# Optimization experiments

Hardware: AMD Instinct MI355X
Metric: run time of the kernel (lower is better)

The kernel has to match this reference:

```python
import jax, jax.numpy as jnp
import numpy as np

N_V, N_H, T, B = 1024, 512, 128, 256


def setup_inputs() -> dict:
    key = jax.random.key(0)
    k = jax.random.split(key, 3)
    v_data = (jax.random.uniform(k[0], (N_V, T, B)) < 0.5).astype(jnp.float32)  # binary visibles
    W = 0.01 * jax.random.normal(k[1], (N_H, N_V), jnp.float32)
    U = 0.01 * jax.random.normal(k[2], (N_H, N_H), jnp.float32)
    b_h = jnp.zeros((N_H,), jnp.float32)
    b_init = jnp.zeros((N_H,), jnp.float32)
    b_v = jnp.zeros((N_V,), jnp.float32)
    return {"v_data": v_data, "W": W, "U": U, "b_h": b_h, "b_init": b_init,
            "b_v": b_v, "CDk": 2}


def _sample_r_over_time(v, W, U, b_h, b_init):
    # v: (V,T,B) -> r: (H,T,B). Sequential mean-field recurrence over T
    # (RTRBM._sample_r_given_v_over_time: t=0 uses b_init and U=0, t>0 uses U,b_h).
    Wv = jnp.einsum('hv,vtb->thb', W, v)  # (T,H,B)
    r0 = jax.nn.sigmoid(Wv[0] + b_init[:, None])

    def step(r_lag, wv_t):
        r_t = jax.nn.sigmoid(wv_t + U @ r_lag + b_h[:, None])
        return r_t, r_t

    _, rs = jax.lax.scan(step, r0, Wv[1:])
    r = jnp.concatenate([r0[None], rs], axis=0)  # (T,H,B)
    return jnp.transpose(r, (1, 0, 2))  # (H,T,B)


def _parallel_r(v, r_lagged, W, U, b_h, b_init):
    # RTRBM._parallel_sample_r_h_given_v probabilities; v:(V,T,B), r_lagged:(H,T,B)
    r0 = jax.nn.sigmoid(jnp.einsum('hv,vb->hb', W, v[:, 0]) + b_init[:, None])
    rr = jax.nn.sigmoid(jnp.einsum('hv,vtb->htb', W, v[:, 1:])
                        + jnp.einsum('hr,rtb->htb', U, r_lagged[:, :-1])
                        + b_h[:, None, None])
    return jnp.concatenate([r0[:, None], rr], axis=1)  # (H,T,B)


def reference(v_data, W, U, b_h, b_init, b_v, CDk):
    key = jax.random.key(42)
    r_data = _sample_r_over_time(v_data, W, U, b_h, b_init)
    key, sk = jax.random.split(key)
    h_model = jax.random.bernoulli(sk, _parallel_r(v_data, r_data, W, U, b_h, b_init)).astype(v_data.dtype)
    for _ in range(CDk - 1):  # CD-k Gibbs chain (CDk is a concrete Python int)
        key, k1, k2 = jax.random.split(key, 3)
        v_prob = jax.nn.sigmoid(jnp.einsum('hv,htb->vtb', W, h_model) + b_v[:, None, None])
        v_model = jax.random.bernoulli(k1, v_prob).astype(v_data.dtype)
        h_model = jax.random.bernoulli(k2, _parallel_r(v_model, r_data, W, U, b_h, b_init)).astype(v_data.dtype)
    key, kf = jax.random.split(key)
    v_model = jax.random.bernoulli(
        kf, jax.nn.sigmoid(jnp.einsum('hv,htb->vtb', W, h_model) + b_v[:, None, None])
    ).astype(v_data.dtype)
    return (v_model, r_data)
```

## Files before the change

### kernel.cpp

```cpp
#include <hip/hip_runtime.h>
#include <stdint.h>

typedef unsigned long long u64;
typedef uint32_t u32;

#define NV 1024
#define NH 512
#define TT 128
#define BB 256
#define TBsz (TT*BB)
#define HTBsz (NH*TBsz)
#define VTBsz (NV*TBsz)
#define NWV (NV/64)
#define NWH (NH/64)
#define QCAP 1048576u
#define DELTA 5e-4
#define BTILE 2

__host__ __device__ inline void tf2x32(uint32_t k0, uint32_t k1,
                                       uint32_t x0, uint32_t x1,
                                       uint32_t& o0, uint32_t& o1) {
  const uint32_t ks2 = k0 ^ k1 ^ 0x1BD11BDAu;
#define ROTL(x,d) (((x)<<(d))|((x)>>(32-(d))))
#define RND(r) { x0 += x1; x1 = ROTL(x1,r); x1 ^= x0; }
  x0 += k0;  x1 += k1;
  RND(13) RND(15) RND(26) RND(6)
  x0 += k1;  x1 += ks2 + 1u;
  RND(17) RND(29) RND(16) RND(24)
  x0 += ks2; x1 += k0 + 2u;
  RND(13) RND(15) RND(26) RND(6)
  x0 += k0;  x1 += k1 + 3u;
  RND(17) RND(29) RND(16) RND(24)
  x0 += k1;  x1 += ks2 + 4u;
  RND(13) RND(15) RND(26) RND(6)
  x0 += ks2; x1 += k0 + 5u;
  o0 = x0; o1 = x1;
#undef RND
#undef ROTL
}

__device__ inline double tf_uniform64(uint32_t k0, uint32_t k1, uint32_t i) {
  uint32_t o0, o1;
  tf2x32(k0, k1, 0u, i, o0, o1);
  uint32_t bits = o0 ^ o1;
  uint32_t fb = (bits >> 9) | 0x3f800000u;
  float f = __uint_as_float(fb) - 1.0f;
  return (double)f;
}

__device__ inline double sigmoid64(double x) { return 1.0 / (1.0 + exp(-x)); }

__global__ __launch_bounds__(256) void kcvt(const float* __restrict__ s,
                                            double* __restrict__ d, int n) {
  int i = blockIdx.x * 256 + threadIdx.x;
  if (i < n) d[i] = (double)s[i];
}

__global__ __launch_bounds__(256) void kprepU(const float* __restrict__ U,
                                              float4* __restrict__ UB) {
  int i = blockIdx.x * 256 + threadIdx.x;
  int r4 = i / NH;
  int h  = i % NH;
  const float* __restrict__ p = U + (size_t)h*NH + r4*4;
  UB[i] = make_float4(p[0], p[1], p[2], p[3]);
}

__global__ __launch_bounds__(256) void kpack_f32(const float* __restrict__ in,
                                                 u64* __restrict__ out) {
  int tb = blockIdx.x * 256 + threadIdx.x;
  for (int w = 0; w < NWV; ++w) {
    u64 m = 0;
    #pragma unroll 8
    for (int j = 0; j < 64; ++j)
      m |= (u64)(in[(size_t)(w*64 + j)*TBsz + tb] != 0.0f ? 1 : 0) << j;
    out[(size_t)tb*NWV + w] = m;
  }
}

__global__ __launch_bounds__(256) void kWv(const u64* __restrict__ vb,
                                           const double* __restrict__ W64,
                                           double* __restrict__ WvT) {
  const int HM = 8;
  int t  = blockIdx.x / (NH/HM);
  int h0 = (blockIdx.x % (NH/HM)) * HM;
  int tb = t*BB + threadIdx.x;
  u64 m[NWV];
  #pragma unroll
  for (int w = 0; w < NWV; ++w) m[w] = vb[(size_t)tb*NWV + w];
  double acc[HM];
  #pragma unroll
  for (int i = 0; i < HM; ++i) acc[i] = 0.0;
  for (int w = 0; w < NWV; ++w) {
    u64 mw = m[w];
    #pragma unroll 8
    for (int j = 0; j < 64; ++j) {
      double bd = (double)((unsigned)((mw >> j) & 1ull));
      int v = w*64 + j;
      #pragma unroll
      for (int i = 0; i < HM; ++i)
        acc[i] = fma(bd, W64[(size_t)(h0+i)*NV + v], acc[i]);
    }
  }
  #pragma unroll
  for (int i = 0; i < HM; ++i)
    WvT[(size_t)tb*NH + h0 + i] = acc[i];
}

__global__ __launch_bounds__(512) void krecur(const double* __restrict__ WvT,
                                              const float4* __restrict__ UB,
                                              const float* __restrict__ bh,
                                              const float* __restrict__ binit,
                                              double* __restrict__ rT) {
  __shared__ double rA[BTILE][NH];
  const int b0 = blockIdx.x * BTILE;
  const int h = threadIdx.x;
  const double bhd = (double)bh[h];
  const double bid = (double)binit[h];
  #pragma unroll
  for (int j = 0; j < BTILE; ++j) {
    double p = sigmoid64(WvT[(size_t)(b0+j)*NH + h] + bid);
    rA[j][h] = p;
    rT[(size_t)(b0+j)*NH + h] = p;
  }
  __syncthreads();
  for (int t = 1; t < TT; ++t) {
    double acc[BTILE], a0[BTILE], a1[BTILE], a2[BTILE], a3[BTILE];
    #pragma unroll
    for (int j = 0; j < BTILE; ++j) {
      acc[j] = WvT[((size_t)t*BB + b0 + j)*NH + h];
      a0[j] = a1[j] = a2[j] = a3[j] = 0.0;
    }
    #pragma unroll 4
    for (int r = 0; r < NH; r += 4) {
      float4 u4 = UB[(size_t)(r >> 2)*NH + h];
      double ux = (double)u4.x, uy = (double)u4.y,
             uz = (double)u4.z, uw = (double)u4.w;
      #pragma unroll
      for (int j = 0; j < BTILE; ++j) {
        a0[j] = fma(ux, rA[j][r+0], a0[j]);
        a1[j] = fma(uy, rA[j][r+1], a1[j]);
        a2[j] = fma(uz, rA[j][r+2], a2[j]);
        a3[j] = fma(uw, rA[j][r+3], a3[j]);
      }
    }
    __syncthreads();
    #pragma unroll
    for (int j = 0; j < BTILE; ++j) {
      double p = sigmoid64((acc[j] + ((a0[j]+a1[j])+(a2[j]+a3[j]))) + bhd);
      rA[j][h] = p;
      rT[((size_t)t*BB + b0 + j)*NH + h] = p;
    }
    __syncthreads();
  }
}

__global__ __launch_bounds__(256) void ktrans(const double* __restrict__ rT,
                                              float* __restrict__ out_r) {
  __shared__ double lds[32][33];
  int t  = blockIdx.x;
  int h0 = blockIdx.y * 32;
  int b0 = blockIdx.z * 32;
  int tx = threadIdx.x & 31;
  int ty = threadIdx.x >> 5;
  #pragma unroll
  for (int i = 0; i < 4; ++i) {
    int row = ty*4 + i;
    lds[row][tx] = rT[((size_t)t*BB + b0 + row)*NH + h0 + tx];
  }
  __syncthreads();
  #pragma unroll
  for (int i = 0; i < 4; ++i) {
    int row = ty*4 + i;
    out_r[(size_t)(h0+row)*TBsz + (size_t)t*BB + b0 + tx] = (float)lds[tx][row];
  }
}

__global__ __launch_bounds__(256) void ksample8(const double* __restrict__ rT,
                                                uint8_t* __restrict__ hbytes,
                                                u32 k0, u32 k1) {
  int i  = blockIdx.x * 256 + threadIdx.x;
  int tb = i >> 6;
  int hw = i & 63;
  int t = tb / BB, b = tb % BB;
  const double* __restrict__ rp = rT + ((size_t)t*BB + b)*NH + hw*8;
  unsigned byte = 0;
  #pragma unroll
  for (int j = 0; j < 8; ++j) {
    double p = rp[j];
    double u = tf_uniform64(k0, k1, (u32)((hw*8 + j)*TBsz + tb));
    byte |= (u < p) ? (1u << j) : 0u;
  }
  hbytes[(size_t)tb*(NH/8) + hw] = (uint8_t)byte;
}

__global__ __launch_bounds__(256) void kvis32(
    const float* __restrict__ W, const float* __restrict__ bv,
    const u64* __restrict__ hbits, uint8_t* __restrict__ vbytes,
    float* __restrict__ vf, u32* __restrict__ queue, u32* __restrict__ cnt,
    u32 k0, u32 k1) {
  const int VM = 8;
  int t  = blockIdx.x / (NV/VM);
  int v0 = (blockIdx.x % (NV/VM)) * VM;
  int tb = t*BB + threadIdx.x;
  u64 hb[NWH];
  #pragma unroll
  for (int w = 0; w < NWH; ++w) hb[w] = hbits[(size_t)tb*NWH + w];
  float acc[VM];
  #pragma unroll
  for (int i = 0; i < VM; ++i) acc[i] = 0.f;
  for (int w = 0; w < NWH; ++w) {
    u64 mw = hb[w];
    #pragma unroll 8
    for (int j = 0; j < 64; ++j) {
      float bd = (float)((u32)((mw >> j) & 1ull));
      const float* __restrict__ Wp = W + (size_t)(w*64 + j)*NV + v0;
      #pragma unroll
      for (int i = 0; i < VM; ++i) acc[i] = fmaf(bd, Wp[i], acc[i]);
    }
  }
  unsigned byte = 0;
  #pragma unroll
  for (int i = 0; i < VM; ++i) {
    float p = 1.f / (1.f + __expf(-(acc[i] + bv[v0+i])));
    size_t o = (size_t)(v0+i)*TBsz + tb;
    double u = tf_uniform64(k0, k1, (u32)o);
    double diff = (double)p - u;
    unsigned smp = diff > 0.0 ? 1u : 0u;
    if (fabs(diff) < DELTA) {
      u32 s = atomicAdd(cnt, 1u);
      if (s < QCAP) queue[s] = (u32)o;
    }
    byte |= smp << i;
    if (vf) vf[o] = (float)smp;
  }
  if (vbytes) vbytes[(size_t)tb*(NV/8) + (v0 >> 3)] = (uint8_t)byte;
}

__global__ __launch_bounds__(256) void kvis_fix(
    const float* __restrict__ W, const float* __restrict__ bv,
    const u64* __restrict__ hbits, u64* __restrict__ fixbits,
    float* __restrict__ vf, const u32* __restrict__ queue,
    const u32* __restrict__ cnt, u32 k0, u32 k1) {
  u32 n = *cnt; if (n > QCAP) n = QCAP;
  for (u32 q = blockIdx.x*256 + threadIdx.x; q < n; q += gridDim.x*256) {
    u32 o = queue[q];
    u32 v = o / TBsz, tb = o % TBsz;
    double a0=0, a1=0, a2=0, a3=0;
    for (int w = 0; w < NWH; ++w) {
      u64 mw = hbits[(size_t)tb*NWH + w];
      for (int j = 0; j < 64; j += 4) {
        if ((mw >> (j+0)) & 1ull) a0 += (double)W[(size_t)(w*64+j+0)*NV + v];
        if ((mw >> (j+1)) & 1ull) a1 += (double)W[(size_t)(w*64+j+1)*NV + v];
        if ((mw >> (j+2)) & 1ull) a2 += (double)W[(size_t)(w*64+j+2)*NV + v];
        if ((mw >> (j+3)) & 1ull) a3 += (double)W[(size_t)(w*64+j+3)*NV + v];
      }
    }
    double p = sigmoid64(((a0+a1)+(a2+a3)) + (double)bv[v]);
    double u = tf_uniform64(k0, k1, o);
    unsigned smp = (u < p) ? 1u : 0u;
    if (vf) vf[o] = (float)smp;
    if (fixbits) {
      size_t wi = (size_t)tb*NWV + (v >> 6);
      unsigned bit = v & 63u;
      unsigned cur = (unsigned)((fixbits[wi] >> bit) & 1ull);
      if (cur != smp) atomicXor(&fixbits[wi], 1ull << bit);
    }
  }
}

__global__ __launch_bounds__(256) void khid32(
    const u64* __restrict__ vbits, const float* __restrict__ W,
    const float* __restrict__ U, const float* __restrict__ bh,
    const float* __restrict__ binit, const float* __restrict__ r32,
    uint8_t* __restrict__ hbytes, u32* __restrict__ queue,
    u32* __restrict__ cnt, u32 k0, u32 k1) {
  const int HM = 8;
  int t  = blockIdx.x / (NH/HM);
  int h0 = (blockIdx.x % (NH/HM)) * HM;
  int tb = t*BB + threadIdx.x;
  u64 m[NWV];
  #pragma unroll
  for (int w = 0; w < NWV; ++w) m[w] = vbits[(size_t)tb*NWV + w];
  float acc[HM];
  #pragma unroll
  for (int i = 0; i < HM; ++i) acc[i] = 0.f;
  for (int w = 0; w < NWV; ++w) {
    u64 mw = m[w];
    #pragma unroll 8
    for (int j = 0; j < 64; ++j) {
      float bd = (float)((u32)((mw >> j) & 1ull));
      int v = w*64 + j;
      #pragma unroll
      for (int i = 0; i < HM; ++i)
        acc[i] = fmaf(bd, W[(size_t)(h0+i)*NV + v], acc[i]);
    }
  }
  if (t > 0) {
    const float* __restrict__ rp = r32 + (size_t)(t-1)*BB + threadIdx.x;
    #pragma unroll 4
    for (int r = 0; r < NH; ++r) {
      float rv = rp[(size_t)r*TBsz];
      #pragma unroll
      for (int i = 0; i < HM; ++i)
        acc[i] = fmaf(U[(size_t)(h0+i)*NH + r], rv, acc[i]);
    }
    #pragma unroll
    for (int i = 0; i < HM; ++i) acc[i] += bh[h0+i];
  } else {
    #pragma unroll
    for (int i = 0; i < HM; ++i) acc[i] += binit[h0+i];
  }
  unsigned byte = 0;
  #pragma unroll
  for (int i = 0; i < HM; ++i) {
    float p = 1.f / (1.f + __expf(-acc[i]));
    size_t o = (size_t)(h0+i)*TBsz + tb;
    double u = tf_uniform64(k0, k1, (u32)o);
    double diff = (double)p - u;
    unsigned smp = diff > 0.0 ? 1u : 0u;
    if (fabs(diff) < DELTA) {
      u32 s = atomicAdd(cnt, 1u);
      if (s < QCAP) queue[s] = (u32)o;
    }
    byte |= smp << i;
  }
  hbytes[(size_t)tb*(NH/8) + (h0 >> 3)] = (uint8_t)byte;
}

__global__ __launch_bounds__(256) void khid_fix(
    const u64* __restrict__ vbits, const float* __restrict__ W,
    const double* __restrict__ U64, const float* __restrict__ bh,
    const float* __restrict__ binit, const double* __restrict__ rT,
    u64* __restrict__ fixbits, const u32* __restrict__ queue,
    const u32* __restrict__ cnt, u32 k0, u32 k1) {
  u32 n = *cnt; if (n > QCAP) n = QCAP;
  for (u32 q = blockIdx.x*256 + threadIdx.x; q < n; q += gridDim.x*256) {
    u32 o = queue[q];
    u32 h = o / TBsz, tb = o % TBsz;
    u32 t = tb / BB, b = tb % BB;
    double a0=0, a1=0, a2=0, a3=0;
    for (int w = 0; w < NWV; ++w) {
      u64 mw = vbits[(size_t)tb*NWV + w];
      for (int j = 0; j < 64; j += 4) {
        if ((mw >> (j+0)) & 1ull) a0 += (double)W[(size_t)h*NV + w*64+j+0];
        if ((mw >> (j+1)) & 1ull) a1 += (double)W[(size_t)h*NV + w*64+j+1];
        if ((mw >> (j+2)) & 1ull) a2 += (double)W[(size_t)h*NV + w*64+j+2];
        if ((mw >> (j+3)) & 1ull) a3 += (double)W[(size_t)h*NV + w*64+j+3];
      }
    }
    double logit = (a0+a1) + (a2+a3);
    if (t > 0) {
      const double* __restrict__ rp = rT + ((size_t)(t-1)*BB + b)*NH;
      const double* __restrict__ Ur = U64 + (size_t)h*NH;
      double u0=0, u1=0, u2=0, u3=0;
      for (int r = 0; r < NH; r += 4) {
        u0 = fma(Ur[r+0], rp[r+0], u0);
        u1 = fma(Ur[r+1], rp[r+1], u1);
        u2 = fma(Ur[r+2], rp[r+2], u2);
        u3 = fma(Ur[r+3], rp[r+3], u3);
      }
      logit = (logit + ((u0+u1)+(u2+u3))) + (double)bh[h];
    } else {
      logit += (double)binit[h];
    }
    double p = sigmoid64(logit);
    double u = tf_uniform64(k0, k1, o);
    unsigned smp = (u < p) ? 1u : 0u;
    size_t wi = (size_t)tb*NWH + (h >> 6);
    unsigned bit = h & 63u;
    unsigned cur = (unsigned)((fixbits[wi] >> bit) & 1ull);
    if (cur != smp) atomicXor(&fixbits[wi], 1ull << bit);
  }
}

extern "C" void kernel_launch(void* const* d_in, const int* in_sizes, int n_in,
                              void* d_out, int out_size, void* d_ws, size_t ws_size,
                              hipStream_t stream) {
  const float* vd    = (const float*)d_in[0];
  const float* W     = (const float*)d_in[1];
  const float* U     = (const float*)d_in[2];
  const float* bh    = (const float*)d_in[3];
  const float* binit = (const float*)d_in[4];
  const float* bv    = (const float*)d_in[5];

  float* out_v = (float*)d_out;
  float* out_r = (float*)d_out + VTBsz;
  double* WvT = (double*)d_out;

  char* w = (char*)d_ws;
  double* rT    = (double*)w;  w += (size_t)HTBsz*8;
  u64* vdbits   = (u64*)w;     w += (size_t)TBsz*NWV*8;
  u64* v1bits   = (u64*)w;     w += (size_t)TBsz*NWV*8;
  u64* h1bits   = (u64*)w;     w += (size_t)TBsz*NWH*8;
  u64* h2bits   = (u64*)w;     w += (size_t)TBsz*NWH*8;
  double* W64   = (double*)w;  w += (size_t)NH*NV*8;
  double* U64   = (double*)w;  w += (size_t)NH*NH*8;
  float4* UB    = (float4*)w;  w += (size_t)NH*NH*4;
  u32* q0       = (u32*)w;     w += (size_t)QCAP*4;
  u32* q1       = (u32*)w;     w += (size_t)QCAP*4;
  u32* q2       = (u32*)w;     w += (size_t)QCAP*4;
  u32* cnt      = (u32*)w;     w += 256;
  (void)ws_size; (void)in_sizes; (void)n_in; (void)out_size;

  uint32_t ka0,ka1, sk0,sk1;
  tf2x32(0u,42u, 0u,0u, ka0,ka1);
  tf2x32(0u,42u, 0u,1u, sk0,sk1);
  uint32_t kb0,kb1, k10,k11, k20,k21;
  tf2x32(ka0,ka1, 0u,0u, kb0,kb1);
  tf2x32(ka0,ka1, 0u,1u, k10,k11);
  tf2x32(ka0,ka1, 0u,2u, k20,k21);
  uint32_t kc0,kc1, kf0,kf1;
  tf2x32(kb0,kb1, 0u,0u, kc0,kc1);
  tf2x32(kb0,kb1, 0u,1u, kf0,kf1);

  hipMemsetAsync(cnt, 0, 3*sizeof(u32), stream);

  kcvt<<<(NH*NV+255)/256, 256, 0, stream>>>(W, W64, NH*NV);
  kcvt<<<(NH*NH+255)/256, 256, 0, stream>>>(U, U64, NH*NH);
  kprepU<<<(NH*NH/4)/256, 256, 0, stream>>>(U, UB);
  kpack_f32<<<TBsz/256, 256, 0, stream>>>(vd, vdbits);

  kWv<<<TT*(NH/8), 256, 0, stream>>>(vdbits, W64, WvT);

  krecur<<<BB/BTILE, NH, 0, stream>>>(WvT, UB, bh, binit, rT);

  ktrans<<<dim3(TT, NH/32, BB/32), 256, 0, stream>>>(rT, out_r);

  ksample8<<<(TBsz*64)/256, 256, 0, stream>>>(rT, (uint8_t*)h1bits, sk0, sk1);

  kvis32<<<TT*(NV/8), 256, 0, stream>>>(W, bv, h1bits, (uint8_t*)v1bits, nullptr,
                                        q0, cnt+0, k10, k11);
  kvis_fix<<<128, 256, 0, stream>>>(W, bv, h1bits, v1bits, nullptr,
                                    q0, cnt+0, k10, k11);

  khid32<<<TT*(NH/8), 256, 0, stream>>>(v1bits, W, U, bh, binit, out_r,
                                        (uint8_t*)h2bits, q1, cnt+1, k20, k21);
  khid_fix<<<128, 256, 0, stream>>>(v1bits, W, U64, bh, binit, rT,
                                    h2bits, q1, cnt+1, k20, k21);

  kvis32<<<TT*(NV/8), 256, 0, stream>>>(W, bv, h2bits, nullptr, out_v,
                                        q2, cnt+2, kf0, kf1);
  kvis_fix<<<128, 256, 0, stream>>>(W, bv, h2bits, nullptr, out_v,
                                    q2, cnt+2, kf0, kf1);
}
```

Baseline: 5.168 ms.

## Split recurrence batch tile across threads and vectorize W loads in Wv and hidden kernels

The recurrence kernel now launches one thread per (hidden unit, batch column) pair, 1024 threads per block, instead of having each thread loop over two batch columns. Its shared-memory reads of r become double2. Separately, the kWv and khid32 inner loops load W as double2 or float4 so one wide load feeds several FMAs. These aim to shorten the serial dependency chain in the time recurrence and cut the number of load instructions. The cost is that each U element is now loaded once per batch column rather than shared across the tile, which raises global/L2 traffic for U.

```diff
diff --git a/kernel.cpp b/kernel.cpp
--- a/kernel.cpp
+++ b/kernel.cpp
@@ -90,15 +90,20 @@
   double acc[HM];
   #pragma unroll
   for (int i = 0; i < HM; ++i) acc[i] = 0.0;
+  const double2* __restrict__ W2 = (const double2*)W64;
   for (int w = 0; w < NWV; ++w) {
     u64 mw = m[w];
     #pragma unroll 8
-    for (int j = 0; j < 64; ++j) {
-      double bd = (double)((unsigned)((mw >> j) & 1ull));
-      int v = w*64 + j;
+    for (int j2 = 0; j2 < 32; ++j2) {
+      double bd0 = (double)((unsigned)((mw >> (2*j2+0)) & 1ull));
+      double bd1 = (double)((unsigned)((mw >> (2*j2+1)) & 1ull));
+      int vi = w*32 + j2;
       #pragma unroll
-      for (int i = 0; i < HM; ++i)
-        acc[i] = fma(bd, W64[(size_t)(h0+i)*NV + v], acc[i]);
+      for (int i = 0; i < HM; ++i) {
+        double2 wv = W2[(size_t)(h0+i)*(NV/2) + vi];
+        acc[i] = fma(bd0, wv.x, acc[i]);
+        acc[i] = fma(bd1, wv.y, acc[i]);
+      }
     }
   }
   #pragma unroll
@@ -106,50 +111,40 @@
     WvT[(size_t)tb*NH + h0 + i] = acc[i];
 }
 
-__global__ __launch_bounds__(512) void krecur(const double* __restrict__ WvT,
-                                              const float4* __restrict__ UB,
-                                              const float* __restrict__ bh,
-                                              const float* __restrict__ binit,
-                                              double* __restrict__ rT) {
+__global__ __launch_bounds__(1024) void krecur(const double* __restrict__ WvT,
+                                               const float4* __restrict__ UB,
+                                               const float* __restrict__ bh,
+                                               const float* __restrict__ binit,
+                                               double* __restrict__ rT) {
   __shared__ double rA[BTILE][NH];
   const int b0 = blockIdx.x * BTILE;
-  const int h = threadIdx.x;
+  const int h = threadIdx.x & (NH-1);
+  const int j = threadIdx.x >> 9;
   const double bhd = (double)bh[h];
-  const double bid = (double)binit[h];
-  #pragma unroll
-  for (int j = 0; j < BTILE; ++j) {
-    double p = sigmoid64(WvT[(size_t)(b0+j)*NH + h] + bid);
+  {
+    double p = sigmoid64(WvT[(size_t)(b0+j)*NH + h] + (double)binit[h]);
     rA[j][h] = p;
     rT[(size_t)(b0+j)*NH + h] = p;
   }
   __syncthreads();
   for (int t = 1; t < TT; ++t) {
-    double acc[BTILE], a0[BTILE], a1[BTILE], a2[BTILE], a3[BTILE];
-    #pragma unroll
-    for (int j = 0; j < BTILE; ++j) {
-      acc[j] = WvT[((size_t)t*BB + b0 + j)*NH + h];
-      a0[j] = a1[j] = a2[j] = a3[j] = 0.0;
-    }
+    double acc = WvT[((size_t)t*BB + b0 + j)*NH + h];
+    double a0=0, a1=0, a2=0, a3=0;
+    const double2* __restrict__ rA2 = (const double2*)rA[j];
     #pragma unroll 4
     for (int r = 0; r < NH; r += 4) {
       float4 u4 = UB[(size_t)(r >> 2)*NH + h];
-      double ux = (double)u4.x, uy = (double)u4.y,
-             uz = (double)u4.z, uw = (double)u4.w;
-      #pragma unroll
-      for (int j = 0; j < BTILE; ++j) {
-        a0[j] = fma(ux, rA[j][r+0], a0[j]);
-        a1[j] = fma(uy, rA[j][r+1], a1[j]);
-        a2[j] = fma(uz, rA[j][r+2], a2[j]);
-        a3[j] = fma(uw, rA[j][r+3], a3[j]);
-      }
+      double2 q01 = rA2[(r>>1)+0];
+      double2 q23 = rA2[(r>>1)+1];
+      a0 = fma((double)u4.x, q01.x, a0);
+      a1 = fma((double)u4.y, q01.y, a1);
+      a2 = fma((double)u4.z, q23.x, a2);
+      a3 = fma((double)u4.w, q23.y, a3);
     }
     __syncthreads();
-    #pragma unroll
-    for (int j = 0; j < BTILE; ++j) {
-      double p = sigmoid64((acc[j] + ((a0[j]+a1[j])+(a2[j]+a3[j]))) + bhd);
-      rA[j][h] = p;
-      rT[((size_t)t*BB + b0 + j)*NH + h] = p;
-    }
+    double p = sigmoid64((acc + ((a0+a1)+(a2+a3))) + bhd);
+    rA[j][h] = p;
+    rT[((size_t)t*BB + b0 + j)*NH + h] = p;
     __syncthreads();
   }
 }
@@ -284,15 +279,24 @@
   float acc[HM];
   #pragma unroll
   for (int i = 0; i < HM; ++i) acc[i] = 0.f;
+  const float4* __restrict__ W4 = (const float4*)W;
   for (int w = 0; w < NWV; ++w) {
     u64 mw = m[w];
-    #pragma unroll 8
-    for (int j = 0; j < 64; ++j) {
-      float bd = (float)((u32)((mw >> j) & 1ull));
-      int v = w*64 + j;
+    #pragma unroll 4
+    for (int j4 = 0; j4 < 16; ++j4) {
+      float bd0 = (float)((u32)((mw >> (4*j4+0)) & 1ull));
+      float bd1 = (float)((u32)((mw >> (4*j4+1)) & 1ull));
+      float bd2 = (float)((u32)((mw >> (4*j4+2)) & 1ull));
+      float bd3 = (float)((u32)((mw >> (4*j4+3)) & 1ull));
+      int vi = w*16 + j4;
       #pragma unroll
-      for (int i = 0; i < HM; ++i)
-        acc[i] = fmaf(bd, W[(size_t)(h0+i)*NV + v], acc[i]);
+      for (int i = 0; i < HM; ++i) {
+        float4 wv = W4[(size_t)(h0+i)*(NV/4) + vi];
+        acc[i] = fmaf(bd0, wv.x, acc[i]);
+        acc[i] = fmaf(bd1, wv.y, acc[i]);
+        acc[i] = fmaf(bd2, wv.z, acc[i]);
+        acc[i] = fmaf(bd3, wv.w, acc[i]);
+      }
     }
   }
   if (t > 0) {
@@ -422,7 +426,7 @@
 
   kWv<<<TT*(NH/8), 256, 0, stream>>>(vdbits, W64, WvT);
 
-  krecur<<<BB/BTILE, NH, 0, stream>>>(WvT, UB, bh, binit, rT);
+  krecur<<<BB/BTILE, NH*BTILE, 0, stream>>>(WvT, UB, bh, binit, rT);
 
   ktrans<<<dim3(TT, NH/32, BB/32), 256, 0, stream>>>(rT, out_r);
 
```

Measured after the change: 5.869 ms. +13.6%, slower.
